# Kernel tuning notes

Measured on AMD Instinct MI355X. Metric: run time of the kernel, lower is better.

## Reference

```python
import jax, jax.numpy as jnp
import numpy as np

B, L, W = 4, 512, 256
VOCAB, E, H = 30000, 300, 768
N_LABELS = 6


def setup_inputs() -> dict:
    key = jax.random.key(0)
    ks = jax.random.split(key, 7)
    return {
        "word_seq": jax.random.randint(ks[0], (B, W), 0, VOCAB),
        "hidden_state": jax.random.normal(ks[1], (B, L, H), dtype=jnp.float32),
        "label_value_matrix": jax.random.randint(ks[2], (B, L, W), 0, N_LABELS),
        "emb_a": jax.random.normal(ks[3], (VOCAB, E), dtype=jnp.float32) * 0.02,
        "lin_w": jax.random.normal(ks[4], (E, H), dtype=jnp.float32) * 0.02,
        "lin_b": jax.random.normal(ks[5], (H,), dtype=jnp.float32) * 0.02,
        "emb_c": jax.random.normal(ks[6], (N_LABELS, H), dtype=jnp.float32) * 0.02,
    }


def reference(word_seq, hidden_state, label_value_matrix, emb_a, lin_w, lin_b, emb_c):
    temper = jnp.asarray(emb_c.shape[1], hidden_state.dtype) ** 0.5  # hidden_size ** 0.5
    # embedding_a lookup + linear projection: [B,W,E] -> [B,W,H]
    a = emb_a[word_seq] @ lin_w + lin_b
    # attention-style scores u = hidden_state @ a^T / temper : [B,L,W]
    u = jnp.einsum("blh,bwh->blw", hidden_state, a) / temper
    # masked exp-normalize WITHOUT max-subtraction (faithful to original)
    mask = jnp.clip(label_value_matrix, 0, 1).astype(u.dtype)
    delta_exp_u = jnp.exp(u) * mask
    p = delta_exp_u / (jnp.sum(delta_exp_u, axis=2, keepdims=True) + 1e-10)
    # embedding_c gather [B,L,W,H], weight by p and reduce over W -> [B,L,H]
    ec = emb_c[label_value_matrix]
    o = jnp.einsum("blw,blwh->blh", p, ec)
    return o
```

## Files before the change

### kernel.cpp

```cpp
#include <hip/hip_runtime.h>

#define BB 4
#define LL 512
#define WW 256
#define EE 300
#define HH 768

typedef __attribute__((ext_vector_type(8))) short bf16x8;
typedef __attribute__((ext_vector_type(4))) float f32x4;

__device__ __forceinline__ short f2bf(float f) {
    union { float f; unsigned u; } v; v.f = f;
    unsigned r = (v.u + 0x7FFFu + ((v.u >> 16) & 1u)) >> 16;
    return (short)r;
}

__global__ __launch_bounds__(256) void k1_a_gemm(
    const int*   __restrict__ word_seq,
    const float* __restrict__ emb_a,
    const float* __restrict__ lin_w,
    const float* __restrict__ lin_b,
    short*       __restrict__ aT)
{
    __shared__ short ea[2][64 * 40];
    __shared__ short lw[2][64 * 40];
    __shared__ int   word[64];

    const int t  = threadIdx.x;
    const int m0 = (blockIdx.x & 15) * 64;
    const int n0 = (blockIdx.x >> 4) * 64;

    if (t < 64) word[t] = word_seq[m0 + t];
    __syncthreads();

    const int lane = t & 63, wv = t >> 6;
    const int l15 = lane & 15, l4 = lane >> 4;

    const int r_ea  = t >> 2;
    const int ec    = (t & 3) * 8;
    const int h_lw  = t & 63;
    const int kc_lw = (t >> 6) * 8;

    const long ea_base = (long)word[r_ea] * EE + ec;

    float ea_reg[8], lw_reg[8];
    {
#pragma unroll
        for (int j = 0; j < 8; j += 2) {
            const float2 p = *(const float2*)(emb_a + ea_base + j);
            ea_reg[j] = p.x; ea_reg[j + 1] = p.y;
        }
#pragma unroll
        for (int j = 0; j < 8; ++j)
            lw_reg[j] = lin_w[(long)(kc_lw + j) * HH + n0 + h_lw];
    }

    f32x4 acc[4] = {};

#pragma unroll
    for (int it = 0; it < 10; ++it) {
        const int cur = it & 1;
        {
            bf16x8 sv;
#pragma unroll
            for (int j = 0; j < 8; ++j) sv[j] = f2bf(ea_reg[j]);
            *(bf16x8*)(&ea[cur][r_ea * 40 + ec]) = sv;
#pragma unroll
            for (int j = 0; j < 8; ++j) sv[j] = f2bf(lw_reg[j]);
            *(bf16x8*)(&lw[cur][h_lw * 40 + kc_lw]) = sv;
        }
        __syncthreads();
        if (it < 9) {
            const int e0 = (it + 1) * 32;
#pragma unroll
            for (int j = 0; j < 8; j += 2) {
                const int e = e0 + ec + j;
                if (e < EE) {
                    const float2 p = *(const float2*)(emb_a + ea_base + e0 + j);
                    ea_reg[j] = p.x; ea_reg[j + 1] = p.y;
                } else { ea_reg[j] = 0.f; ea_reg[j + 1] = 0.f; }
            }
#pragma unroll
            for (int j = 0; j < 8; ++j) {
                const int e = e0 + kc_lw + j;
                lw_reg[j] = (e < EE) ? lin_w[(long)e * HH + n0 + h_lw] : 0.f;
            }
        }
        {
            const bf16x8 af = *(const bf16x8*)(&ea[cur][(wv * 16 + l15) * 40 + l4 * 8]);
#pragma unroll
            for (int nf = 0; nf < 4; ++nf) {
                const bf16x8 bfv = *(const bf16x8*)(&lw[cur][(nf * 16 + l15) * 40 + l4 * 8]);
                acc[nf] = __builtin_amdgcn_mfma_f32_16x16x32_bf16(af, bfv, acc[nf], 0, 0, 0);
            }
        }
    }

    const int b = m0 >> 8;
#pragma unroll
    for (int nf = 0; nf < 4; ++nf) {
        const int h    = n0 + nf * 16 + l15;
        const float bv = lin_b[h];
        const long hbase = ((long)(b * 96 + (h >> 3)) * 256) * 8 + (h & 7);
#pragma unroll
        for (int i = 0; i < 4; ++i) {
            const int w = (m0 & 255) + wv * 16 + l4 * 4 + i;
            aT[hbase + (long)w * 8] = f2bf(acc[nf][i] + bv);
        }
    }
}

__global__ __launch_bounds__(256) void k2_attn(
    const float* __restrict__ hidden,
    const int*   __restrict__ label,
    const short* __restrict__ aT,
    const float* __restrict__ emb_c,
    float*       __restrict__ out)
{
    __shared__ short hid[16 * 776];
    __shared__ float s_lds[4][16][5];
    __shared__ float s_fin[16][5];
    __shared__ float invd[16];

    const int t = threadIdx.x, lane = t & 63, wv = t >> 6;
    const int l15 = lane & 15, l4 = lane >> 4;
    const int bl0 = blockIdx.x * 16;
    const int b   = bl0 >> 9;

    {
        const float* hrow = hidden + (long)bl0 * HH;
#pragma unroll
        for (int j = 0; j < 6; ++j) {
            const int idx = (t + j * 256) * 8;
            const int row = idx / HH;
            const int col = idx - row * HH;
            const float4 p0 = *(const float4*)(hrow + idx);
            const float4 p1 = *(const float4*)(hrow + idx + 4);
            bf16x8 v;
            v[0] = f2bf(p0.x); v[1] = f2bf(p0.y); v[2] = f2bf(p0.z); v[3] = f2bf(p0.w);
            v[4] = f2bf(p1.x); v[5] = f2bf(p1.y); v[6] = f2bf(p1.z); v[7] = f2bf(p1.w);
            *(bf16x8*)(&hid[row * 776 + col]) = v;
        }
    }
    __syncthreads();

    const short* abase = aT + (long)b * 96 * 256 * 8;
    f32x4 acc[4] = {};

#pragma unroll
    for (int ks = 0; ks < 24; ++ks) {
        const bf16x8 af = *(const bf16x8*)(&hid[l15 * 776 + ks * 32 + l4 * 8]);
#pragma unroll
        for (int nf = 0; nf < 4; ++nf) {
            const int w = wv * 64 + nf * 16 + l15;
            const bf16x8 bfv =
                *(const bf16x8*)(abase + ((long)(ks * 4 + l4) * 256 + w) * 8);
            acc[nf] = __builtin_amdgcn_mfma_f32_16x16x32_bf16(af, bfv, acc[nf], 0, 0, 0);
        }
    }

    const float inv_temper = 0.03608439182435161f;
    float s_loc[4][5];
#pragma unroll
    for (int i = 0; i < 4; ++i)
#pragma unroll
        for (int c = 0; c < 5; ++c) s_loc[i][c] = 0.f;

    const int* lab_base = label + (long)bl0 * WW;
#pragma unroll
    for (int nf = 0; nf < 4; ++nf) {
        const int w = wv * 64 + nf * 16 + l15;
#pragma unroll
        for (int i = 0; i < 4; ++i) {
            const int row = l4 * 4 + i;
            const int lv  = lab_base[row * WW + w];
            const float e = __expf(acc[nf][i] * inv_temper);
#pragma unroll
            for (int c = 1; c <= 5; ++c)
                s_loc[i][c - 1] += (lv == c) ? e : 0.f;
        }
    }
#pragma unroll
    for (int i = 0; i < 4; ++i) {
#pragma unroll
        for (int c = 0; c < 5; ++c) {
            float v = s_loc[i][c];
            v += __shfl_xor(v, 1);
            v += __shfl_xor(v, 2);
            v += __shfl_xor(v, 4);
            v += __shfl_xor(v, 8);
            s_loc[i][c] = v;
        }
    }
    if (l15 == 0) {
#pragma unroll
        for (int i = 0; i < 4; ++i)
#pragma unroll
            for (int c = 0; c < 5; ++c)
                s_lds[wv][l4 * 4 + i][c] = s_loc[i][c];
    }
    __syncthreads();
    if (t < 16) {
        float den = 0.f;
#pragma unroll
        for (int c = 0; c < 5; ++c) {
            const float s = s_lds[0][t][c] + s_lds[1][t][c] +
                            s_lds[2][t][c] + s_lds[3][t][c];
            s_fin[t][c] = s;
            den += s;
        }
        invd[t] = 1.0f / (den + 1e-10f);
    }
    __syncthreads();

    float ecv[3][5];
#pragma unroll
    for (int q = 0; q < 3; ++q)
#pragma unroll
        for (int c = 0; c < 5; ++c)
            ecv[q][c] = emb_c[(c + 1) * HH + t + q * 256];

    float* obase = out + (long)bl0 * HH;
    for (int row = 0; row < 16; ++row) {
        const float id = invd[row];
        const float s0 = s_fin[row][0], s1 = s_fin[row][1], s2 = s_fin[row][2],
                    s3 = s_fin[row][3], s4 = s_fin[row][4];
#pragma unroll
        for (int q = 0; q < 3; ++q) {
            const float v = s0 * ecv[q][0] + s1 * ecv[q][1] + s2 * ecv[q][2] +
                            s3 * ecv[q][3] + s4 * ecv[q][4];
            obase[(long)row * HH + t + q * 256] = v * id;
        }
    }
}

extern "C" void kernel_launch(void* const* d_in, const int* in_sizes, int n_in,
                              void* d_out, int out_size, void* d_ws, size_t ws_size,
                              hipStream_t stream) {
    const int*   word_seq = (const int*)  d_in[0];
    const float* hidden   = (const float*)d_in[1];
    const int*   label    = (const int*)  d_in[2];
    const float* emb_a    = (const float*)d_in[3];
    const float* lin_w    = (const float*)d_in[4];
    const float* lin_b    = (const float*)d_in[5];
    const float* emb_c    = (const float*)d_in[6];
    float* out = (float*)d_out;
    short* aT  = (short*)d_ws;

    k1_a_gemm<<<dim3(192), 256, 0, stream>>>(word_seq, emb_a, lin_w, lin_b, aT);
    k2_attn<<<dim3(128), 256, 0, stream>>>(hidden, label, aT, emb_c, out);
}
```

Measured before the change: 27.39 us.

## Fuse projection GEMM and attention kernels with a software grid barrier

The two kernel launches are merged into one persistent-style kernel of 256 blocks. The first 192 blocks compute the projected embedding GEMM into workspace, and every block stages its hidden rows into LDS. A grid-wide atomic barrier then separates this phase from the attention phase, which now covers 8 rows per block instead of 16 and zero-pads the other half of each MFMA tile. This removes a launch gap and overlaps the hidden-state load with the GEMM, at the cost of a memset, spin-waiting, wasted MFMA work on padded rows, and a co-residency assumption for the barrier.

```diff
diff --git a/kernel.cpp b/kernel.cpp
--- a/kernel.cpp
+++ b/kernel.cpp
@@ -15,122 +15,137 @@
     return (short)r;
 }
 
-__global__ __launch_bounds__(256) void k1_a_gemm(
+__device__ __forceinline__ void grid_barrier(int* cnt, int* flag, int nblocks) {
+    __syncthreads();
+    if (threadIdx.x == 0) {
+        __threadfence();
+        const int old = __hip_atomic_fetch_add(cnt, 1, __ATOMIC_ACQ_REL,
+                                               __HIP_MEMORY_SCOPE_AGENT);
+        if (old == nblocks - 1) {
+            __hip_atomic_store(flag, 1, __ATOMIC_RELEASE, __HIP_MEMORY_SCOPE_AGENT);
+        } else {
+            while (__hip_atomic_load(flag, __ATOMIC_RELAXED,
+                                     __HIP_MEMORY_SCOPE_AGENT) == 0) {
+                __builtin_amdgcn_s_sleep(2);
+            }
+        }
+        __threadfence();
+    }
+    __syncthreads();
+}
+
+__global__ __launch_bounds__(256) void fused_gca(
     const int*   __restrict__ word_seq,
+    const float* __restrict__ hidden,
+    const int*   __restrict__ label,
     const float* __restrict__ emb_a,
     const float* __restrict__ lin_w,
     const float* __restrict__ lin_b,
-    short*       __restrict__ aT)
+    const float* __restrict__ emb_c,
+    float*       __restrict__ out,
+    short*       __restrict__ aT,
+    int*         __restrict__ bar)
 {
     __shared__ short ea[2][64 * 40];
     __shared__ short lw[2][64 * 40];
     __shared__ int   word[64];
-
-    const int t  = threadIdx.x;
-    const int m0 = (blockIdx.x & 15) * 64;
-    const int n0 = (blockIdx.x >> 4) * 64;
-
-    if (t < 64) word[t] = word_seq[m0 + t];
-    __syncthreads();
-
-    const int lane = t & 63, wv = t >> 6;
-    const int l15 = lane & 15, l4 = lane >> 4;
-
-    const int r_ea  = t >> 2;
-    const int ec    = (t & 3) * 8;
-    const int h_lw  = t & 63;
-    const int kc_lw = (t >> 6) * 8;
-
-    const long ea_base = (long)word[r_ea] * EE + ec;
-
-    float ea_reg[8], lw_reg[8];
-    {
-#pragma unroll
-        for (int j = 0; j < 8; j += 2) {
-            const float2 p = *(const float2*)(emb_a + ea_base + j);
-            ea_reg[j] = p.x; ea_reg[j + 1] = p.y;
-        }
-#pragma unroll
-        for (int j = 0; j < 8; ++j)
-            lw_reg[j] = lin_w[(long)(kc_lw + j) * HH + n0 + h_lw];
-    }
-
-    f32x4 acc[4] = {};
-
-#pragma unroll
-    for (int it = 0; it < 10; ++it) {
-        const int cur = it & 1;
-        {
-            bf16x8 sv;
-#pragma unroll
-            for (int j = 0; j < 8; ++j) sv[j] = f2bf(ea_reg[j]);
-            *(bf16x8*)(&ea[cur][r_ea * 40 + ec]) = sv;
-#pragma unroll
-            for (int j = 0; j < 8; ++j) sv[j] = f2bf(lw_reg[j]);
-            *(bf16x8*)(&lw[cur][h_lw * 40 + kc_lw]) = sv;
-        }
-        __syncthreads();
-        if (it < 9) {
-            const int e0 = (it + 1) * 32;
-#pragma unroll
-            for (int j = 0; j < 8; j += 2) {
-                const int e = e0 + ec + j;
-                if (e < EE) {
-                    const float2 p = *(const float2*)(emb_a + ea_base + e0 + j);
-                    ea_reg[j] = p.x; ea_reg[j + 1] = p.y;
-                } else { ea_reg[j] = 0.f; ea_reg[j + 1] = 0.f; }
-            }
-#pragma unroll
-            for (int j = 0; j < 8; ++j) {
-                const int e = e0 + kc_lw + j;
-                lw_reg[j] = (e < EE) ? lin_w[(long)e * HH + n0 + h_lw] : 0.f;
-            }
-        }
-        {
-            const bf16x8 af = *(const bf16x8*)(&ea[cur][(wv * 16 + l15) * 40 + l4 * 8]);
-#pragma unroll
-            for (int nf = 0; nf < 4; ++nf) {
-                const bf16x8 bfv = *(const bf16x8*)(&lw[cur][(nf * 16 + l15) * 40 + l4 * 8]);
-                acc[nf] = __builtin_amdgcn_mfma_f32_16x16x32_bf16(af, bfv, acc[nf], 0, 0, 0);
-            }
-        }
-    }
-
-    const int b = m0 >> 8;
-#pragma unroll
-    for (int nf = 0; nf < 4; ++nf) {
-        const int h    = n0 + nf * 16 + l15;
-        const float bv = lin_b[h];
-        const long hbase = ((long)(b * 96 + (h >> 3)) * 256) * 8 + (h & 7);
-#pragma unroll
-        for (int i = 0; i < 4; ++i) {
-            const int w = (m0 & 255) + wv * 16 + l4 * 4 + i;
-            aT[hbase + (long)w * 8] = f2bf(acc[nf][i] + bv);
-        }
-    }
-}
-
-__global__ __launch_bounds__(256) void k2_attn(
-    const float* __restrict__ hidden,
-    const int*   __restrict__ label,
-    const short* __restrict__ aT,
-    const float* __restrict__ emb_c,
-    float*       __restrict__ out)
-{
     __shared__ short hid[16 * 776];
     __shared__ float s_lds[4][16][5];
     __shared__ float s_fin[16][5];
     __shared__ float invd[16];
 
-    const int t = threadIdx.x, lane = t & 63, wv = t >> 6;
+    const int bid = blockIdx.x;
+    const int t   = threadIdx.x;
+    const int lane = t & 63, wv = t >> 6;
     const int l15 = lane & 15, l4 = lane >> 4;
-    const int bl0 = blockIdx.x * 16;
-    const int b   = bl0 >> 9;
-
+
+    if (bid < 192) {
+        const int m0 = (bid & 15) * 64;
+        const int n0 = (bid >> 4) * 64;
+
+        if (t < 64) word[t] = word_seq[m0 + t];
+        __syncthreads();
+
+        const int r_ea  = t >> 2;
+        const int ec    = (t & 3) * 8;
+        const int h_lw  = t & 63;
+        const int kc_lw = (t >> 6) * 8;
+
+        const long ea_base = (long)word[r_ea] * EE + ec;
+
+        float ea_reg[8], lw_reg[8];
+        {
+#pragma unroll
+            for (int j = 0; j < 8; j += 2) {
+                const float2 p = *(const float2*)(emb_a + ea_base + j);
+                ea_reg[j] = p.x; ea_reg[j + 1] = p.y;
+            }
+#pragma unroll
+            for (int j = 0; j < 8; ++j)
+                lw_reg[j] = lin_w[(long)(kc_lw + j) * HH + n0 + h_lw];
+        }
+
+        f32x4 acc[4] = {};
+
+#pragma unroll
+        for (int it = 0; it < 10; ++it) {
+            const int cur = it & 1;
+            {
+                bf16x8 sv;
+#pragma unroll
+                for (int j = 0; j < 8; ++j) sv[j] = f2bf(ea_reg[j]);
+                *(bf16x8*)(&ea[cur][r_ea * 40 + ec]) = sv;
+#pragma unroll
+                for (int j = 0; j < 8; ++j) sv[j] = f2bf(lw_reg[j]);
+                *(bf16x8*)(&lw[cur][h_lw * 40 + kc_lw]) = sv;
+            }
+            __syncthreads();
+            if (it < 9) {
+                const int e0 = (it + 1) * 32;
+#pragma unroll
+                for (int j = 0; j < 8; j += 2) {
+                    const int e = e0 + ec + j;
+                    if (e < EE) {
+                        const float2 p = *(const float2*)(emb_a + ea_base + e0 + j);
+                        ea_reg[j] = p.x; ea_reg[j + 1] = p.y;
+                    } else { ea_reg[j] = 0.f; ea_reg[j + 1] = 0.f; }
+                }
+#pragma unroll
+                for (int j = 0; j < 8; ++j) {
+                    const int e = e0 + kc_lw + j;
+                    lw_reg[j] = (e < EE) ? lin_w[(long)e * HH + n0 + h_lw] : 0.f;
+                }
+            }
+            {
+                const bf16x8 af = *(const bf16x8*)(&ea[cur][(wv * 16 + l15) * 40 + l4 * 8]);
+#pragma unroll
+                for (int nf = 0; nf < 4; ++nf) {
+                    const bf16x8 bfv = *(const bf16x8*)(&lw[cur][(nf * 16 + l15) * 40 + l4 * 8]);
+                    acc[nf] = __builtin_amdgcn_mfma_f32_16x16x32_bf16(af, bfv, acc[nf], 0, 0, 0);
+                }
+            }
+        }
+
+        const int b1 = m0 >> 8;
+#pragma unroll
+        for (int nf = 0; nf < 4; ++nf) {
+            const int h    = n0 + nf * 16 + l15;
+            const float bv = lin_b[h];
+            const long hbase = ((long)(b1 * 96 + (h >> 3)) * 256) * 8 + (h & 7);
+#pragma unroll
+            for (int i = 0; i < 4; ++i) {
+                const int w = (m0 & 255) + wv * 16 + l4 * 4 + i;
+                aT[hbase + (long)w * 8] = f2bf(acc[nf][i] + bv);
+            }
+        }
+    }
+
+    const int row0 = bid * 8;
+    const int b    = row0 >> 9;
     {
-        const float* hrow = hidden + (long)bl0 * HH;
-#pragma unroll
-        for (int j = 0; j < 6; ++j) {
+        const float* hrow = hidden + (long)row0 * HH;
+#pragma unroll
+        for (int j = 0; j < 3; ++j) {
             const int idx = (t + j * 256) * 8;
             const int row = idx / HH;
             const int col = idx - row * HH;
@@ -141,95 +156,105 @@
             v[4] = f2bf(p1.x); v[5] = f2bf(p1.y); v[6] = f2bf(p1.z); v[7] = f2bf(p1.w);
             *(bf16x8*)(&hid[row * 776 + col]) = v;
         }
-    }
-    __syncthreads();
-
-    const short* abase = aT + (long)b * 96 * 256 * 8;
-    f32x4 acc[4] = {};
-
-#pragma unroll
-    for (int ks = 0; ks < 24; ++ks) {
-        const bf16x8 af = *(const bf16x8*)(&hid[l15 * 776 + ks * 32 + l4 * 8]);
+        const bf16x8 z = {};
+#pragma unroll
+        for (int j = 0; j < 3; ++j) {
+            const int idx = (t + j * 256) * 8;
+            const int row = idx / HH;
+            const int col = idx - row * HH;
+            *(bf16x8*)(&hid[(8 + row) * 776 + col]) = z;
+        }
+    }
+
+    grid_barrier(bar, bar + 8, 256);
+
+    {
+        const short* abase = aT + (long)b * 96 * 256 * 8;
+        f32x4 acc[4] = {};
+#pragma unroll
+        for (int ks = 0; ks < 24; ++ks) {
+            const bf16x8 af = *(const bf16x8*)(&hid[l15 * 776 + ks * 32 + l4 * 8]);
+#pragma unroll
+            for (int nf = 0; nf < 4; ++nf) {
+                const int w = wv * 64 + nf * 16 + l15;
+                const bf16x8 bfv =
+                    *(const bf16x8*)(abase + ((long)(ks * 4 + l4) * 256 + w) * 8);
+                acc[nf] = __builtin_amdgcn_mfma_f32_16x16x32_bf16(af, bfv, acc[nf], 0, 0, 0);
+            }
+        }
+
+        const float inv_temper = 0.03608439182435161f;
+        float s_loc[4][5];
+#pragma unroll
+        for (int i = 0; i < 4; ++i)
+#pragma unroll
+            for (int c = 0; c < 5; ++c) s_loc[i][c] = 0.f;
+
+        const int* lab_base = label + (long)row0 * WW;
 #pragma unroll
         for (int nf = 0; nf < 4; ++nf) {
             const int w = wv * 64 + nf * 16 + l15;
-            const bf16x8 bfv =
-                *(const bf16x8*)(abase + ((long)(ks * 4 + l4) * 256 + w) * 8);
-            acc[nf] = __builtin_amdgcn_mfma_f32_16x16x32_bf16(af, bfv, acc[nf], 0, 0, 0);
-        }
-    }
-
-    const float inv_temper = 0.03608439182435161f;
-    float s_loc[4][5];
-#pragma unroll
-    for (int i = 0; i < 4; ++i)
-#pragma unroll
-        for (int c = 0; c < 5; ++c) s_loc[i][c] = 0.f;
-
-    const int* lab_base = label + (long)bl0 * WW;
-#pragma unroll
-    for (int nf = 0; nf < 4; ++nf) {
-        const int w = wv * 64 + nf * 16 + l15;
+#pragma unroll
+            for (int i = 0; i < 4; ++i) {
+                const int row = l4 * 4 + i;
+                const int lv  = (row < 8) ? lab_base[row * WW + w] : 0;
+                const float e = __expf(acc[nf][i] * inv_temper);
+#pragma unroll
+                for (int c = 1; c <= 5; ++c)
+                    s_loc[i][c - 1] += (lv == c) ? e : 0.f;
+            }
+        }
 #pragma unroll
         for (int i = 0; i < 4; ++i) {
-            const int row = l4 * 4 + i;
-            const int lv  = lab_base[row * WW + w];
-            const float e = __expf(acc[nf][i] * inv_temper);
-#pragma unroll
-            for (int c = 1; c <= 5; ++c)
-                s_loc[i][c - 1] += (lv == c) ? e : 0.f;
-        }
-    }
-#pragma unroll
-    for (int i = 0; i < 4; ++i) {
-#pragma unroll
-        for (int c = 0; c < 5; ++c) {
-            float v = s_loc[i][c];
-            v += __shfl_xor(v, 1);
-            v += __shfl_xor(v, 2);
-            v += __shfl_xor(v, 4);
-            v += __shfl_xor(v, 8);
-            s_loc[i][c] = v;
-        }
-    }
-    if (l15 == 0) {
-#pragma unroll
-        for (int i = 0; i < 4; ++i)
+#pragma unroll
+            for (int c = 0; c < 5; ++c) {
+                float v = s_loc[i][c];
+                v += __shfl_xor(v, 1);
+                v += __shfl_xor(v, 2);
+                v += __shfl_xor(v, 4);
+                v += __shfl_xor(v, 8);
+                s_loc[i][c] = v;
+            }
+        }
+        if (l15 == 0) {
+#pragma unroll
+            for (int i = 0; i < 4; ++i)
+#pragma unroll
+                for (int c = 0; c < 5; ++c)
+                    s_lds[wv][l4 * 4 + i][c] = s_loc[i][c];
+        }
+        __syncthreads();
+        if (t < 8) {
+            float den = 0.f;
+#pragma unroll
+            for (int c = 0; c < 5; ++c) {
+                const float s = s_lds[0][t][c] + s_lds[1][t][c] +
+                                s_lds[2][t][c] + s_lds[3][t][c];
+                s_fin[t][c] = s;
+                den += s;
+            }
+            invd[t] = 1.0f / (den + 1e-10f);
+        }
+        __syncthreads();
+
+        float ecv[3][5];
+#pragma unroll
+        for (int q = 0; q < 3; ++q)
 #pragma unroll
             for (int c = 0; c < 5; ++c)
-                s_lds[wv][l4 * 4 + i][c] = s_loc[i][c];
-    }
-    __syncthreads();
-    if (t < 16) {
-        float den = 0.f;
-#pragma unroll
-        for (int c = 0; c < 5; ++c) {
-            const float s = s_lds[0][t][c] + s_lds[1][t][c] +
-                            s_lds[2][t][c] + s_lds[3][t][c];
-            s_fin[t][c] = s;
-            den += s;
-        }
-        invd[t] = 1.0f / (den + 1e-10f);
-    }
-    __syncthreads();
-
-    float ecv[3][5];
-#pragma unroll
-    for (int q = 0; q < 3; ++q)
-#pragma unroll
-        for (int c = 0; c < 5; ++c)
-            ecv[q][c] = emb_c[(c + 1) * HH + t + q * 256];
-
-    float* obase = out + (long)bl0 * HH;
-    for (int row = 0; row < 16; ++row) {
-        const float id = invd[row];
-        const float s0 = s_fin[row][0], s1 = s_fin[row][1], s2 = s_fin[row][2],
-                    s3 = s_fin[row][3], s4 = s_fin[row][4];
-#pragma unroll
-        for (int q = 0; q < 3; ++q) {
-            const float v = s0 * ecv[q][0] + s1 * ecv[q][1] + s2 * ecv[q][2] +
-                            s3 * ecv[q][3] + s4 * ecv[q][4];
-            obase[(long)row * HH + t + q * 256] = v * id;
+                ecv[q][c] = emb_c[(c + 1) * HH + t + q * 256];
+
+        float* obase = out + (long)row0 * HH;
+        for (int row = 0; row < 8; ++row) {
+            const float id = invd[row];
+            const float s0 = s_fin[row][0], s1 = s_fin[row][1], s2 = s_fin[row][2],
+                        s3 = s_fin[row][3], s4 = s_fin[row][4];
+#pragma unroll
+            for (int q = 0; q < 3; ++q) {
+                const float v = s0 * ecv[q][0] + s1 * ecv[q][1] + s2 * ecv[q][2] +
+                                s3 * ecv[q][3] + s4 * ecv[q][4];
+                obase[(long)row * HH + t + q * 256] = v * id;
+            }
         }
     }
 }
@@ -245,8 +270,11 @@
     const float* lin_b    = (const float*)d_in[5];
     const float* emb_c    = (const float*)d_in[6];
     float* out = (float*)d_out;
+
     short* aT  = (short*)d_ws;
-
-    k1_a_gemm<<<dim3(192), 256, 0, stream>>>(word_seq, emb_a, lin_w, lin_b, aT);
-    k2_attn<<<dim3(128), 256, 0, stream>>>(hidden, label, aT, emb_c, out);
-}
+    int*   bar = (int*)((char*)d_ws + 0x180000);
+
+    hipMemsetAsync((void*)bar, 0, 256, stream);
+    fused_gca<<<dim3(256), 256, 0, stream>>>(word_seq, hidden, label, emb_a,
+                                             lin_w, lin_b, emb_c, out, aT, bar);
+}
```

After: 49.80 us. 81.8% more time.

## Split attention over W halves, add output kernel, restage K1 in two halves

Applied to the files above, without the earlier changes.

The first GEMM now loads its operands in two large halves of 160 columns each. This replaces the ten small 32-wide double-buffered steps, giving fewer barriers and wider float4 loads at the cost of many more registers. The attention kernel is split across two W halves, which doubles the grid to 256 blocks to fill more CUs. Its partial per-label sums go to workspace, and a new third kernel combines them, normalizes and writes the output. The trade is an extra kernel launch and a small round trip through global memory in exchange for more parallelism.

```diff
diff --git a/kernel.cpp b/kernel.cpp
--- a/kernel.cpp
+++ b/kernel.cpp
@@ -15,93 +15,97 @@
     return (short)r;
 }
 
-__global__ __launch_bounds__(256) void k1_a_gemm(
+__global__ __launch_bounds__(256, 1) void k1_a_gemm(
     const int*   __restrict__ word_seq,
     const float* __restrict__ emb_a,
     const float* __restrict__ lin_w,
     const float* __restrict__ lin_b,
     short*       __restrict__ aT)
 {
-    __shared__ short ea[2][64 * 40];
-    __shared__ short lw[2][64 * 40];
-    __shared__ int   word[64];
+    __shared__ short eaL[2][64 * 168];
+    __shared__ short lwL[2][64 * 168];
 
     const int t  = threadIdx.x;
     const int m0 = (blockIdx.x & 15) * 64;
     const int n0 = (blockIdx.x >> 4) * 64;
 
-    if (t < 64) word[t] = word_seq[m0 + t];
-    __syncthreads();
-
     const int lane = t & 63, wv = t >> 6;
     const int l15 = lane & 15, l4 = lane >> 4;
 
-    const int r_ea  = t >> 2;
-    const int ec    = (t & 3) * 8;
-    const int h_lw  = t & 63;
-    const int kc_lw = (t >> 6) * 8;
-
-    const long ea_base = (long)word[r_ea] * EE + ec;
-
-    float ea_reg[8], lw_reg[8];
-    {
-#pragma unroll
-        for (int j = 0; j < 8; j += 2) {
-            const float2 p = *(const float2*)(emb_a + ea_base + j);
-            ea_reg[j] = p.x; ea_reg[j + 1] = p.y;
-        }
-#pragma unroll
-        for (int j = 0; j < 8; ++j)
-            lw_reg[j] = lin_w[(long)(kc_lw + j) * HH + n0 + h_lw];
-    }
+    const int r_ea = t >> 2;
+    const int q_ea = t & 3;
+    const int h_lw = t & 63;
+    const int q_lw = t >> 6;
+
+    const int  wrow    = word_seq[m0 + r_ea];
+    const float* arow  = emb_a + (long)wrow * EE;
 
     f32x4 acc[4] = {};
 
-#pragma unroll
-    for (int it = 0; it < 10; ++it) {
-        const int cur = it & 1;
+    float ea_reg[40], lw_reg[40];
+
+#pragma unroll
+    for (int half = 0; half < 2; ++half) {
+        const int k0 = half * 160;
         {
-            bf16x8 sv;
-#pragma unroll
-            for (int j = 0; j < 8; ++j) sv[j] = f2bf(ea_reg[j]);
-            *(bf16x8*)(&ea[cur][r_ea * 40 + ec]) = sv;
-#pragma unroll
-            for (int j = 0; j < 8; ++j) sv[j] = f2bf(lw_reg[j]);
-            *(bf16x8*)(&lw[cur][h_lw * 40 + kc_lw]) = sv;
+            const int cbase = k0 + q_ea * 40;
+#pragma unroll
+            for (int c4 = 0; c4 < 10; ++c4) {
+                const int col = cbase + c4 * 4;
+                if (col <= 296) {
+                    const float4 p = *(const float4*)(arow + col);
+                    ea_reg[c4 * 4 + 0] = p.x; ea_reg[c4 * 4 + 1] = p.y;
+                    ea_reg[c4 * 4 + 2] = p.z; ea_reg[c4 * 4 + 3] = p.w;
+                } else {
+                    ea_reg[c4 * 4 + 0] = 0.f; ea_reg[c4 * 4 + 1] = 0.f;
+                    ea_reg[c4 * 4 + 2] = 0.f; ea_reg[c4 * 4 + 3] = 0.f;
+                }
+            }
+            const int cb2 = k0 + q_lw * 40;
+#pragma unroll
+            for (int j = 0; j < 40; ++j) {
+                const int col = cb2 + j;
+                lw_reg[j] = (col < EE) ? lin_w[(long)col * HH + n0 + h_lw] : 0.f;
+            }
+        }
+        {
+            const int eoff = r_ea * 168 + q_ea * 40;
+#pragma unroll
+            for (int c8 = 0; c8 < 5; ++c8) {
+                bf16x8 sv;
+#pragma unroll
+                for (int j = 0; j < 8; ++j) sv[j] = f2bf(ea_reg[c8 * 8 + j]);
+                *(bf16x8*)(&eaL[half][eoff + c8 * 8]) = sv;
+            }
+            const int loff = h_lw * 168 + q_lw * 40;
+#pragma unroll
+            for (int c8 = 0; c8 < 5; ++c8) {
+                bf16x8 sv;
+#pragma unroll
+                for (int j = 0; j < 8; ++j) sv[j] = f2bf(lw_reg[c8 * 8 + j]);
+                *(bf16x8*)(&lwL[half][loff + c8 * 8]) = sv;
+            }
         }
         __syncthreads();
-        if (it < 9) {
-            const int e0 = (it + 1) * 32;
-#pragma unroll
-            for (int j = 0; j < 8; j += 2) {
-                const int e = e0 + ec + j;
-                if (e < EE) {
-                    const float2 p = *(const float2*)(emb_a + ea_base + e0 + j);
-                    ea_reg[j] = p.x; ea_reg[j + 1] = p.y;
-                } else { ea_reg[j] = 0.f; ea_reg[j + 1] = 0.f; }
-            }
-#pragma unroll
-            for (int j = 0; j < 8; ++j) {
-                const int e = e0 + kc_lw + j;
-                lw_reg[j] = (e < EE) ? lin_w[(long)e * HH + n0 + h_lw] : 0.f;
-            }
-        }
-        {
-            const bf16x8 af = *(const bf16x8*)(&ea[cur][(wv * 16 + l15) * 40 + l4 * 8]);
+#pragma unroll
+        for (int ks = 0; ks < 5; ++ks) {
+            const bf16x8 af =
+                *(const bf16x8*)(&eaL[half][(wv * 16 + l15) * 168 + ks * 32 + l4 * 8]);
 #pragma unroll
             for (int nf = 0; nf < 4; ++nf) {
-                const bf16x8 bfv = *(const bf16x8*)(&lw[cur][(nf * 16 + l15) * 40 + l4 * 8]);
+                const bf16x8 bfv =
+                    *(const bf16x8*)(&lwL[half][(nf * 16 + l15) * 168 + ks * 32 + l4 * 8]);
                 acc[nf] = __builtin_amdgcn_mfma_f32_16x16x32_bf16(af, bfv, acc[nf], 0, 0, 0);
             }
         }
     }
 
-    const int b = m0 >> 8;
+    const int b1 = m0 >> 8;
 #pragma unroll
     for (int nf = 0; nf < 4; ++nf) {
         const int h    = n0 + nf * 16 + l15;
         const float bv = lin_b[h];
-        const long hbase = ((long)(b * 96 + (h >> 3)) * 256) * 8 + (h & 7);
+        const long hbase = ((long)(b1 * 96 + (h >> 3)) * 256) * 8 + (h & 7);
 #pragma unroll
         for (int i = 0; i < 4; ++i) {
             const int w = (m0 & 255) + wv * 16 + l4 * 4 + i;
@@ -110,22 +114,22 @@
     }
 }
 
-__global__ __launch_bounds__(256) void k2_attn(
+__global__ __launch_bounds__(256, 1) void k2_attn(
     const float* __restrict__ hidden,
     const int*   __restrict__ label,
     const short* __restrict__ aT,
-    const float* __restrict__ emb_c,
-    float*       __restrict__ out)
+    float*       __restrict__ s_part)
 {
     __shared__ short hid[16 * 776];
     __shared__ float s_lds[4][16][5];
-    __shared__ float s_fin[16][5];
-    __shared__ float invd[16];
 
     const int t = threadIdx.x, lane = t & 63, wv = t >> 6;
     const int l15 = lane & 15, l4 = lane >> 4;
-    const int bl0 = blockIdx.x * 16;
-    const int b   = bl0 >> 9;
+    const int blt   = blockIdx.x >> 1;
+    const int whalf = blockIdx.x & 1;
+    const int bl0   = blt * 16;
+    const int b     = bl0 >> 9;
+    const int w0    = whalf * 128;
 
     {
         const float* hrow = hidden + (long)bl0 * HH;
@@ -145,14 +149,14 @@
     __syncthreads();
 
     const short* abase = aT + (long)b * 96 * 256 * 8;
-    f32x4 acc[4] = {};
+    f32x4 acc[2] = {};
 
 #pragma unroll
     for (int ks = 0; ks < 24; ++ks) {
         const bf16x8 af = *(const bf16x8*)(&hid[l15 * 776 + ks * 32 + l4 * 8]);
 #pragma unroll
-        for (int nf = 0; nf < 4; ++nf) {
-            const int w = wv * 64 + nf * 16 + l15;
+        for (int nf = 0; nf < 2; ++nf) {
+            const int w = w0 + wv * 32 + nf * 16 + l15;
             const bf16x8 bfv =
                 *(const bf16x8*)(abase + ((long)(ks * 4 + l4) * 256 + w) * 8);
             acc[nf] = __builtin_amdgcn_mfma_f32_16x16x32_bf16(af, bfv, acc[nf], 0, 0, 0);
@@ -168,8 +172,8 @@
 
     const int* lab_base = label + (long)bl0 * WW;
 #pragma unroll
-    for (int nf = 0; nf < 4; ++nf) {
-        const int w = wv * 64 + nf * 16 + l15;
+    for (int nf = 0; nf < 2; ++nf) {
+        const int w = w0 + wv * 32 + nf * 16 + l15;
 #pragma unroll
         for (int i = 0; i < 4; ++i) {
             const int row = l4 * 4 + i;
@@ -201,17 +205,22 @@
     }
     __syncthreads();
     if (t < 16) {
-        float den = 0.f;
 #pragma unroll
         for (int c = 0; c < 5; ++c) {
             const float s = s_lds[0][t][c] + s_lds[1][t][c] +
                             s_lds[2][t][c] + s_lds[3][t][c];
-            s_fin[t][c] = s;
-            den += s;
-        }
-        invd[t] = 1.0f / (den + 1e-10f);
-    }
-    __syncthreads();
+            s_part[(long)(bl0 + t) * 10 + whalf * 5 + c] = s;
+        }
+    }
+}
+
+__global__ __launch_bounds__(256, 1) void k3_out(
+    const float* __restrict__ s_part,
+    const float* __restrict__ emb_c,
+    float*       __restrict__ out)
+{
+    const int t  = threadIdx.x;
+    const int r0 = blockIdx.x * 8;
 
     float ecv[3][5];
 #pragma unroll
@@ -220,16 +229,21 @@
         for (int c = 0; c < 5; ++c)
             ecv[q][c] = emb_c[(c + 1) * HH + t + q * 256];
 
-    float* obase = out + (long)bl0 * HH;
-    for (int row = 0; row < 16; ++row) {
-        const float id = invd[row];
-        const float s0 = s_fin[row][0], s1 = s_fin[row][1], s2 = s_fin[row][2],
-                    s3 = s_fin[row][3], s4 = s_fin[row][4];
+    for (int r = 0; r < 8; ++r) {
+        const int row = r0 + r;
+        float s[5], den = 1e-10f;
+#pragma unroll
+        for (int c = 0; c < 5; ++c) {
+            s[c] = s_part[(long)row * 10 + c] + s_part[(long)row * 10 + 5 + c];
+            den += s[c];
+        }
+        const float id = 1.0f / den;
+        float* orow = out + (long)row * HH;
 #pragma unroll
         for (int q = 0; q < 3; ++q) {
-            const float v = s0 * ecv[q][0] + s1 * ecv[q][1] + s2 * ecv[q][2] +
-                            s3 * ecv[q][3] + s4 * ecv[q][4];
-            obase[(long)row * HH + t + q * 256] = v * id;
+            const float v = s[0] * ecv[q][0] + s[1] * ecv[q][1] + s[2] * ecv[q][2] +
+                            s[3] * ecv[q][3] + s[4] * ecv[q][4];
+            orow[t + q * 256] = v * id;
         }
     }
 }
@@ -245,8 +259,11 @@
     const float* lin_b    = (const float*)d_in[5];
     const float* emb_c    = (const float*)d_in[6];
     float* out = (float*)d_out;
-    short* aT  = (short*)d_ws;
+
+    short* aT     = (short*)d_ws;
+    float* s_part = (float*)((char*)d_ws + 0x180000);
 
     k1_a_gemm<<<dim3(192), 256, 0, stream>>>(word_seq, emb_a, lin_w, lin_b, aT);
-    k2_attn<<<dim3(128), 256, 0, stream>>>(hidden, label, aT, emb_c, out);
-}
+    k2_attn<<<dim3(256), 256, 0, stream>>>(hidden, label, aT, s_part);
+    k3_out<<<dim3(256), 256, 0, stream>>>(s_part, emb_c, out);
+}
```

New measurement: 24.13 us. -11.9%, faster.
